# Performance work log

Measured on AMD Instinct MI355X. Metric: run time of the kernel, lower is better.

Reference implementation:

```python
import jax, jax.numpy as jnp
import numpy as np

E, C, H, W = 64, 8, 32, 32  # E zonotope rows (1 center + 63 error terms)


def setup_inputs() -> dict:
    key = jax.random.key(0)
    x = jax.random.normal(key, (E, C, H, W), dtype=jnp.float32)
    # Zero center => lower < 0 < upper everywhere, so every element crosses
    # and the number of new error terms equals C*H*W (fixed output shape).
    x = x.at[0].set(0.0)
    return {"x": x}


def reference(x):
    e = x.shape[0]
    content_shape = x.shape[1:]
    n = int(np.prod(content_shape))  # max possible new error terms

    err = jnp.sum(jnp.abs(x[1:]), axis=0)
    upper = x[0] + err
    lower = x[0] - err

    cross = (lower * upper < 0).astype(x.dtype)   # crossing-zero mask
    nonneg = (lower >= 0).astype(x.dtype)         # strictly positive mask

    lam = nonneg + cross * upper / (upper - lower)
    lam = jnp.where(jnp.isnan(lam), 0.5, lam)
    # torch assigns lambda via .data (detached from the autograd graph)
    lam = jax.lax.stop_gradient(lam)

    delta = jnp.maximum(-lam * lower, (1.0 - lam) * upper)

    head = (delta / 2 + lam * x[0]) * cross + x[0] * nonneg          # new center
    body = x[1:] * (lam * cross + nonneg)                            # scaled old error terms

    # Vectorized stream-compaction scatter replacing the scripted .item() loop:
    # element k (flat order) with cross==True goes to tail row cumsum(cross)[k]-1.
    flat_cond = cross.reshape(-1) > 0
    vals = (delta / 2).reshape(-1)
    rows = jnp.cumsum(flat_cond.astype(jnp.int32)) - 1
    rows = jnp.clip(rows, 0, n - 1)
    tail = jnp.zeros((n, n), dtype=x.dtype)
    # (row, col) pairs are unique per column; masked-out elements write 0 (no-op).
    tail = tail.at[rows, jnp.arange(n)].set(jnp.where(flat_cond, vals, 0.0))

    return jnp.concatenate(
        [head[None], body, tail.reshape((n,) + content_shape)], axis=0
    )
```

## Files before the change

kernel.cpp:

```cpp
#include <hip/hip_runtime.h>
#include <math.h>

#define EROWS 64
#define NCOL  8192
#define TAIL_OFF (EROWS * NCOL)
#define TAIL_F4  (NCOL * NCOL / 4)

#define STAT_BLOCKS 256
#define FILL_F4_PER_BLOCK 4096
#define FILL_BLOCKS (TAIL_F4 / FILL_F4_PER_BLOCK)

typedef float vf4 __attribute__((ext_vector_type(4)));
typedef int   vi4 __attribute__((ext_vector_type(4)));

#define WS_VAL(ws)     ((float*)(ws))
#define WS_FLAG(ws)    ((int*)((char*)(ws) + 32768))
#define WS_COLOF(ws)   ((int*)((char*)(ws) + 65536))
#define WS_TAILVAL(ws) ((float*)((char*)(ws) + 98304))
#define WS_COUNT(ws)   ((int*)((char*)(ws) + 131072))

__global__ void fused_kernel(const float* __restrict__ x,
                             float* __restrict__ out,
                             float* __restrict__ val,
                             int* __restrict__ flag) {
    const int tid = threadIdx.x;

    if (blockIdx.x >= STAT_BLOCKS) {
        vf4 z; z.x = 0.f; z.y = 0.f; z.z = 0.f; z.w = 0.f;
        vf4* base = (vf4*)out + (TAIL_OFF / 4)
                  + (size_t)(blockIdx.x - STAT_BLOCKS) * FILL_F4_PER_BLOCK;
        #pragma unroll
        for (int i = 0; i < 16; ++i)
            base[i * 256 + tid] = z;
        return;
    }

    __shared__ float part[256];
    __shared__ float sc[32];

    const int c   = tid & 31;
    const int eg  = tid >> 5;
    const int col = blockIdx.x * 32 + c;

    float xv[8];
    int   ev[8];
    int   n = 0;
    float s = 0.f;
    #pragma unroll
    for (int j = 0; j < 8; ++j) {
        int e = eg + 8 * j;
        if (e == 0) continue;
        float v = x[e * NCOL + col];
        xv[n] = v; ev[n] = e; ++n;
        s += fabsf(v);
    }
    part[eg * 32 + c] = s;
    __syncthreads();

    if (tid < 32) {
        float err = 0.f;
        #pragma unroll
        for (int g = 0; g < 8; ++g)
            err += part[g * 32 + tid];

        int   k  = blockIdx.x * 32 + tid;
        float x0 = x[k];
        float upper = x0 + err;
        float lower = x0 - err;

        float cross  = (lower * upper < 0.f) ? 1.f : 0.f;
        float nonneg = (lower >= 0.f) ? 1.f : 0.f;

        float lam = nonneg + cross * upper / (upper - lower);
        if (isnan(lam)) lam = 0.5f;

        float delta = fmaxf(-lam * lower, (1.f - lam) * upper);

        out[k]   = (delta * 0.5f + lam * x0) * cross + x0 * nonneg;
        val[k]   = delta * 0.5f;
        flag[k]  = (cross > 0.f) ? 1 : 0;
        sc[tid]  = lam * cross + nonneg;
    }
    __syncthreads();

    float scl = sc[c];
    #pragma unroll
    for (int i = 0; i < 8; ++i) {
        if (i < n)
            out[ev[i] * NCOL + col] = xv[i] * scl;
    }
}

__global__ void scan_kernel(const float* __restrict__ val,
                            const int* __restrict__ flag,
                            int* __restrict__ colof,
                            float* __restrict__ tailval,
                            int* __restrict__ count) {
    const int t    = threadIdx.x;
    const int lane = t & 63;
    const int wave = t >> 6;
    const int PER  = NCOL / 256;

    int f[PER];
    int mysum = 0;
    const vi4* fp = (const vi4*)(flag + t * PER);
    for (int j = 0; j < PER / 4; ++j) {
        vi4 v = fp[j];
        f[4*j+0] = v.x; f[4*j+1] = v.y; f[4*j+2] = v.z; f[4*j+3] = v.w;
        mysum += v.x + v.y + v.z + v.w;
    }

    int s = mysum;
    for (int off = 1; off < 64; off <<= 1) {
        int v = __shfl_up(s, off);
        if (lane >= off) s += v;
    }

    __shared__ int wsum[4];
    if (lane == 63) wsum[wave] = s;
    __syncthreads();
    int wbase = 0;
    for (int w = 0; w < wave; ++w) wbase += wsum[w];

    int running = wbase + s - mysum;

    for (int j = 0; j < PER; ++j) {
        int k = t * PER + j;
        if (f[j]) {
            colof[running]   = k;
            tailval[running] = val[k];
            ++running;
        }
    }
    if (t == 255) *count = wsum[0] + wsum[1] + wsum[2] + wsum[3];
}

__global__ void diag_kernel(const int* __restrict__ colof,
                            const float* __restrict__ tailval,
                            const int* __restrict__ count,
                            float* __restrict__ out) {
    int r = blockIdx.x * blockDim.x + threadIdx.x;
    int cnt = *count;
    if (r < cnt)
        out[TAIL_OFF + (size_t)r * NCOL + colof[r]] = tailval[r];
}

extern "C" void kernel_launch(void* const* d_in, const int* in_sizes, int n_in,
                              void* d_out, int out_size, void* d_ws, size_t ws_size,
                              hipStream_t stream) {
    const float* x = (const float*)d_in[0];
    float* out = (float*)d_out;

    fused_kernel<<<STAT_BLOCKS + FILL_BLOCKS, 256, 0, stream>>>(
        x, out, WS_VAL(d_ws), WS_FLAG(d_ws));
    scan_kernel<<<1, 256, 0, stream>>>(WS_VAL(d_ws), WS_FLAG(d_ws),
                                       WS_COLOF(d_ws), WS_TAILVAL(d_ws), WS_COUNT(d_ws));
    diag_kernel<<<NCOL / 256, 256, 0, stream>>>(WS_COLOF(d_ws), WS_TAILVAL(d_ws),
                                                WS_COUNT(d_ws), out);
}
```

Before: 278.0 us.

## Fuse diagonal scatter into tail zero-fill after compaction scan

Moves the tail zero-fill out of the column-stats kernel into a kernel that runs after the scan. Each block writes two tail rows and inserts the compacted diagonal value while writing zeros, which removes the separate scattered diag kernel. The cost is that the large fill can no longer overlap the stats work, and it now waits for the single-block scan.

```diff
diff --git a/kernel.cpp b/kernel.cpp
--- a/kernel.cpp
+++ b/kernel.cpp
@@ -19,21 +19,11 @@
 #define WS_TAILVAL(ws) ((float*)((char*)(ws) + 98304))
 #define WS_COUNT(ws)   ((int*)((char*)(ws) + 131072))
 
-__global__ void fused_kernel(const float* __restrict__ x,
-                             float* __restrict__ out,
-                             float* __restrict__ val,
-                             int* __restrict__ flag) {
+__global__ void colstats_kernel(const float* __restrict__ x,
+                                float* __restrict__ out,
+                                float* __restrict__ val,
+                                int* __restrict__ flag) {
     const int tid = threadIdx.x;
-
-    if (blockIdx.x >= STAT_BLOCKS) {
-        vf4 z; z.x = 0.f; z.y = 0.f; z.z = 0.f; z.w = 0.f;
-        vf4* base = (vf4*)out + (TAIL_OFF / 4)
-                  + (size_t)(blockIdx.x - STAT_BLOCKS) * FILL_F4_PER_BLOCK;
-        #pragma unroll
-        for (int i = 0; i < 16; ++i)
-            base[i * 256 + tid] = z;
-        return;
-    }
 
     __shared__ float part[256];
     __shared__ float sc[32];
@@ -135,14 +125,34 @@
     if (t == 255) *count = wsum[0] + wsum[1] + wsum[2] + wsum[3];
 }
 
-__global__ void diag_kernel(const int* __restrict__ colof,
-                            const float* __restrict__ tailval,
-                            const int* __restrict__ count,
-                            float* __restrict__ out) {
-    int r = blockIdx.x * blockDim.x + threadIdx.x;
-    int cnt = *count;
-    if (r < cnt)
-        out[TAIL_OFF + (size_t)r * NCOL + colof[r]] = tailval[r];
+__global__ void filltail_kernel(const int* __restrict__ colof,
+                                const float* __restrict__ tailval,
+                                const int* __restrict__ count,
+                                float* __restrict__ out) {
+    const int tid = threadIdx.x;
+    const int b   = blockIdx.x;
+    const int cnt = *count;
+
+    const int r0 = 2 * b, r1 = 2 * b + 1;
+    int   c0 = (r0 < cnt) ? colof[r0]   : -1;
+    float v0 = (r0 < cnt) ? tailval[r0] : 0.f;
+    int   c1 = (r1 < cnt) ? colof[r1]   : -1;
+    float v1 = (r1 < cnt) ? tailval[r1] : 0.f;
+
+    vf4* base = (vf4*)out + (TAIL_OFF / 4) + (size_t)b * FILL_F4_PER_BLOCK;
+    #pragma unroll
+    for (int i = 0; i < 16; ++i) {
+        int j   = i * 256 + tid;
+        int col = (i < 8) ? c0 : c1;
+        float tv = (i < 8) ? v0 : v1;
+        int cs  = (j & 2047) << 2;
+        vf4 v;
+        v.x = (col == cs + 0) ? tv : 0.f;
+        v.y = (col == cs + 1) ? tv : 0.f;
+        v.z = (col == cs + 2) ? tv : 0.f;
+        v.w = (col == cs + 3) ? tv : 0.f;
+        base[j] = v;
+    }
 }
 
 extern "C" void kernel_launch(void* const* d_in, const int* in_sizes, int n_in,
@@ -151,10 +161,9 @@
     const float* x = (const float*)d_in[0];
     float* out = (float*)d_out;
 
-    fused_kernel<<<STAT_BLOCKS + FILL_BLOCKS, 256, 0, stream>>>(
-        x, out, WS_VAL(d_ws), WS_FLAG(d_ws));
+    colstats_kernel<<<STAT_BLOCKS, 256, 0, stream>>>(x, out, WS_VAL(d_ws), WS_FLAG(d_ws));
     scan_kernel<<<1, 256, 0, stream>>>(WS_VAL(d_ws), WS_FLAG(d_ws),
                                        WS_COLOF(d_ws), WS_TAILVAL(d_ws), WS_COUNT(d_ws));
-    diag_kernel<<<NCOL / 256, 256, 0, stream>>>(WS_COLOF(d_ws), WS_TAILVAL(d_ws),
-                                                WS_COUNT(d_ws), out);
+    filltail_kernel<<<FILL_BLOCKS, 256, 0, stream>>>(WS_COLOF(d_ws), WS_TAILVAL(d_ws),
+                                                     WS_COUNT(d_ws), out);
 }
```

New measurement: 282.2 us. Within noise of the previous version (+1.5%).
